# Kernel optimization log

Measured on AMD Instinct MI355X. Metric: run time of the kernel, lower is better.

## Reference

```python
import jax, jax.numpy as jnp
import numpy as np

BETA = 0.9
THRESHOLD = 1.0
SLOPE = 25.0


def _heaviside(x):
    return (x > 0).astype(x.dtype)


def setup_inputs() -> dict:
    key = jax.random.key(0)
    k = jax.random.split(key, 5)
    B, T, I, H, C = 256, 500, 256, 512, 8
    x = jax.random.normal(k[0], (B, T, I), dtype=jnp.float32)
    W1 = jax.random.normal(k[1], (H, I), dtype=jnp.float32) * (1.0 / np.sqrt(I))
    b1 = jax.random.normal(k[2], (H,), dtype=jnp.float32) * 0.01
    W2 = jax.random.normal(k[3], (C, H), dtype=jnp.float32) * (1.0 / np.sqrt(H))
    b2 = jax.random.normal(k[4], (C,), dtype=jnp.float32) * 0.01
    return {"x": x, "W1": W1, "b1": b1, "W2": W2, "b2": b2}


def reference(x, W1, b1, W2, b2):
    # x: (B, T, I)
    B, T, I = x.shape
    # Time-invariant fc1 batched outside the recurrence: (B, T, H)
    cur1 = jnp.einsum('bti,hi->bth', x, W1) + b1
    cur1_t = jnp.swapaxes(cur1, 0, 1)  # (T, B, H)

    def step(mem, cur):
        # snntorch Leaky (reset_mechanism='subtract'):
        # reset computed from previous mem crossing threshold
        reset = _heaviside(mem - THRESHOLD)
        mem_new = BETA * mem + cur - reset * THRESHOLD
        spk = _heaviside(mem_new - THRESHOLD)
        return mem_new, spk

    mem0 = jnp.zeros((B, W1.shape[0]), dtype=x.dtype)
    _, spks = jax.lax.scan(step, mem0, cur1_t)  # spks: (T, B, H)

    # out_sum = sum_t (spk_t @ W2^T + b2) = (sum_t spk_t) @ W2^T + T*b2
    spk_sum = spks.sum(axis=0)  # (B, H)
    out_sum = spk_sum @ W2.T + jnp.asarray(T, x.dtype) * b2  # (B, C)
    return out_sum
```

## Files before the change

### kernel.cpp

```cpp
#include <hip/hip_runtime.h>


#define B_   256
#define T_   500
#define I_   256
#define H_   512
#define C_   8

#define TC   128
#define BK   32
#define NKS  8
#define NCH  4
#define NR   (NCH * NKS)

#define WBUF  0
#define XBUF0 32768
#define XBUF1 49152

typedef __attribute__((ext_vector_type(8))) _Float16 half8;
typedef __attribute__((ext_vector_type(2))) __fp16 f16x2;
typedef __attribute__((ext_vector_type(4))) float f32x4;

typedef __attribute__((address_space(1))) const unsigned int as1_uint;
typedef __attribute__((address_space(3))) unsigned int as3_uint;

__device__ __forceinline__ void lds_dma16(const void* g, void* l) {
  __builtin_amdgcn_global_load_lds((as1_uint*)g, (as3_uint*)l, 16, 0, 0);
}

#define MFMA16(A, B, Cc) __builtin_amdgcn_mfma_f32_16x16x32_f16(A, B, Cc, 0, 0, 0)

__global__ void init_out_kernel(const float* __restrict__ b2,
                                float* __restrict__ out) {
  int idx = blockIdx.x * 256 + threadIdx.x;
  if (idx < B_ * C_) out[idx] = (float)T_ * b2[idx & (C_ - 1)];
}

__global__ void split_w1_kernel(const float* __restrict__ W1,
                                char* __restrict__ ws) {
  const int n = blockIdx.x * 256 + threadIdx.x;
  if (n >= H_ * NKS * 4) return;
  const int h = n >> 5, ks = (n >> 2) & 7, c = n & 3;
  const float* src = W1 + h * I_ + ks * BK + c * 8;
  union { half8 v; _Float16 e[8]; } hi, lo;
  #pragma unroll
  for (int e = 0; e < 8; ++e) {
    const float w = 16.0f * src[e];
    const _Float16 wh = (_Float16)w;
    hi.e[e] = wh;
    lo.e[e] = (_Float16)(w - (float)wh);
  }
  const int slot = (((h & 255) << 2) + c) ^ (h & 7);
  char* dst = ws + (size_t)((ks << 1) + (h >> 8)) * 32768 + ((size_t)slot << 4);
  *(half8*)dst = hi.v;
  *(half8*)(dst + 16384) = lo.v;
}

__device__ __forceinline__ void load_x16(const float* xb, int t, int ib,
                                         float* a) {
  if (t < T_) {
    const float* xr = xb + (size_t)t * I_ + ib;
    #pragma unroll
    for (int q = 0; q < 4; ++q) {
      const float4 v = *(const float4*)(xr + 4 * q);
      a[4 * q + 0] = v.x; a[4 * q + 1] = v.y;
      a[4 * q + 2] = v.z; a[4 * q + 3] = v.w;
    }
  } else {
    #pragma unroll
    for (int e = 0; e < 16; ++e) a[e] = 0.f;
  }
}

__device__ __forceinline__ void cvt_store_x(char* dstbase, int xs0, int xs1,
                                            const float* a) {
  union { half8 v; f16x2 p[4]; } h0, h1, l0, l1;
  #pragma unroll
  for (int k = 0; k < 4; ++k) {
    const f16x2 ha = __builtin_amdgcn_cvt_pkrtz(a[2 * k], a[2 * k + 1]);
    h0.p[k] = ha;
    l0.p[k] = __builtin_amdgcn_cvt_pkrtz(a[2 * k] - (float)ha[0],
                                         a[2 * k + 1] - (float)ha[1]);
    const f16x2 hb = __builtin_amdgcn_cvt_pkrtz(a[8 + 2 * k], a[9 + 2 * k]);
    h1.p[k] = hb;
    l1.p[k] = __builtin_amdgcn_cvt_pkrtz(a[8 + 2 * k] - (float)hb[0],
                                         a[9 + 2 * k] - (float)hb[1]);
  }
  *(half8*)(dstbase + xs0) = h0.v;
  *(half8*)(dstbase + xs1) = h1.v;
  *(half8*)(dstbase + 8192 + xs0) = l0.v;
  *(half8*)(dstbase + 8192 + xs1) = l1.v;
}

__global__ __launch_bounds__(256, 2) void snn_mfma2(
    const float* __restrict__ x, const char* __restrict__ ws,
    const float* __restrict__ b1, const float* __restrict__ W2,
    float* __restrict__ out) {
  __shared__ __align__(16) char smem[65536];

  const int tid = threadIdx.x;
  const int b = blockIdx.x, half = blockIdx.y;
  const int l = tid & 63, wv = tid >> 6;
  const int rr = l & 15, cc = l >> 4;

  const float* xb = x + (size_t)b * (T_ * I_);

  const int fsw = (((rr << 2) + cc) ^ (rr & 7)) << 4;

  const int tl = tid >> 1, ih = tid & 1;
  const int xs0 = ((((tl << 2) + ih * 2 + 0) ^ (tl & 7)) << 4);
  const int xs1 = ((((tl << 2) + ih * 2 + 1) ^ (tl & 7)) << 4);

  const float bias16 = 16.0f * b1[half * 256 + wv * 64 + l];
  float mreg = 0.f, cnt = 0.f;

  f32x4 acc[8][4];
  #pragma unroll
  for (int i = 0; i < 8; ++i)
    #pragma unroll
    for (int j = 0; j < 4; ++j) acc[i][j] = (f32x4){0.f, 0.f, 0.f, 0.f};

  {
    const char* wg = ws + (size_t)half * 32768;
    #pragma unroll
    for (int q = 0; q < 8; ++q)
      lds_dma16(wg + (wv * 8 + q) * 1024 + l * 16,
                smem + WBUF + (wv * 8 + q) * 1024);
    float a16[16];
    load_x16(xb, tl, ih * 16, a16);
    cvt_store_x(smem + XBUF0, xs0, xs1, a16);
    __syncthreads();
  }

  #pragma unroll 1
  for (int r = 0; r < NR; ++r) {
    const int ks = r & 7, chunk = r >> 3;
    const int xcur = XBUF0 + (r & 1) * 16384;
    const int xnxt = XBUF0 + ((r + 1) & 1) * 16384;
    const bool do_stage = (r + 1 < NR);

    float a16[16];
    if (do_stage) {
      const int t1 = ((r + 1) >> 3) * TC + tl;
      load_x16(xb, t1, ((r + 1) & 7) * BK + ih * 16, a16);
    }

    half8 ah[8], al[8], bh[4], bl[4];
    #pragma unroll
    for (int i = 0; i < 8; ++i) {
      ah[i] = *(const half8*)(smem + xcur + i * 1024 + fsw);
      al[i] = *(const half8*)(smem + xcur + 8192 + i * 1024 + fsw);
    }
    #pragma unroll
    for (int j = 0; j < 4; ++j) {
      bh[j] = *(const half8*)(smem + WBUF + wv * 4096 + j * 1024 + fsw);
      bl[j] = *(const half8*)(smem + WBUF + 16384 + wv * 4096 + j * 1024 + fsw);
    }
    #pragma unroll
    for (int i = 0; i < 8; ++i)
      #pragma unroll
      for (int j = 0; j < 4; ++j) {
        acc[i][j] = MFMA16(ah[i], bh[j], acc[i][j]);
        acc[i][j] = MFMA16(al[i], bh[j], acc[i][j]);
        acc[i][j] = MFMA16(ah[i], bl[j], acc[i][j]);
      }

    if (ks == 7) {
      asm volatile("" ::: "memory");
      const int t0 = chunk * TC;
      #pragma unroll
      for (int p = 0; p < 4; ++p) {
        #pragma unroll
        for (int i2 = 0; i2 < 2; ++i2) {
          #pragma unroll
          for (int j = 0; j < 4; ++j) {
            const int rl = j * 16 + rr;
            const int g = i2 * 4 + cc;
            const int ad = (rl >> 5) * 16384 + wv * 4096 + (rl & 31) * 128 +
                           ((g ^ (rl & 7)) << 4);
            *(f32x4*)(smem + ad) = acc[2 * p + i2][j];
          }
        }
        const int nt = T_ - (t0 + 32 * p) < 32 ? T_ - (t0 + 32 * p) : 32;
        const int rb = (l >> 5) * 16384 + wv * 4096 + (l & 31) * 128;
        #pragma unroll
        for (int g = 0; g < 8; ++g) {
          if (4 * g < nt) {
            const float4 v =
                *(const float4*)(smem + rb + ((g ^ (l & 7)) << 4));
            const float cv[4] = {v.x, v.y, v.z, v.w};
            #pragma unroll
            for (int e = 0; e < 4; ++e) {
              const float curv = cv[e] + bias16;
              const float rst = (mreg > 16.0f) ? 16.0f : 0.f;
              mreg = fmaf(0.9f, mreg, curv) - rst;
              if (mreg > 16.0f) cnt += 1.f;
            }
          }
        }
      }
      #pragma unroll
      for (int i = 0; i < 8; ++i)
        #pragma unroll
        for (int j = 0; j < 4; ++j) acc[i][j] = (f32x4){0.f, 0.f, 0.f, 0.f};
    }

    __syncthreads();

    if (do_stage) {
      const char* wg = ws + (size_t)((((r + 1) & 7) << 1) + half) * 32768;
      #pragma unroll
      for (int q = 0; q < 8; ++q)
        lds_dma16(wg + (wv * 8 + q) * 1024 + l * 16,
                  smem + WBUF + (wv * 8 + q) * 1024);
      cvt_store_x(smem + xnxt, xs0, xs1, a16);
    }
    __syncthreads();
  }

  const int hglob = half * 256 + wv * 64 + l;
  #pragma unroll
  for (int c = 0; c < C_; ++c) {
    float p = cnt * W2[c * H_ + hglob];
    #pragma unroll
    for (int m = 32; m >= 1; m >>= 1) p += __shfl_xor(p, m, 64);
    if (l == 0) atomicAdd(&out[b * C_ + c], p);
  }
}

extern "C" void kernel_launch(void* const* d_in, const int* in_sizes, int n_in,
                              void* d_out, int out_size, void* d_ws,
                              size_t ws_size, hipStream_t stream) {
  (void)in_sizes; (void)n_in; (void)ws_size; (void)out_size;
  const float* x  = (const float*)d_in[0];
  const float* W1 = (const float*)d_in[1];
  const float* b1 = (const float*)d_in[2];
  const float* W2 = (const float*)d_in[3];
  const float* b2 = (const float*)d_in[4];
  float* out = (float*)d_out;
  char* ws = (char*)d_ws;

  init_out_kernel<<<dim3((B_ * C_ + 255) / 256), dim3(256), 0, stream>>>(b2, out);
  split_w1_kernel<<<dim3(H_ * NKS * 4 / 256), dim3(256), 0, stream>>>(W1, ws);
  snn_mfma2<<<dim3(B_, 2), dim3(256), 0, stream>>>(x, ws, b1, W2, out);
}
```

Measured before the change: 261.2 us.

## Relayout W1 and x tiles to MFMA fragment order and fold bias into accumulators

W1 halves are pre-packed in the order the MFMA B fragments are read, and x tiles are staged so each lane writes and reads a contiguous 16-byte fragment. This removes the XOR swizzle arithmetic and lets the weight DMA use simple linear offsets. The bias is preloaded into the accumulators instead of being added in the scan. The membrane epilogue now processes 16 timesteps at a time through the idle next x buffer and tracks the spike flag in a register rather than re-comparing. Dropping the swizzle risks LDS bank conflicts on the epilogue stores.

```diff
diff --git a/kernel.cpp b/kernel.cpp
--- a/kernel.cpp
+++ b/kernel.cpp
@@ -40,7 +40,10 @@
                                 char* __restrict__ ws) {
   const int n = blockIdx.x * 256 + threadIdx.x;
   if (n >= H_ * NKS * 4) return;
-  const int h = n >> 5, ks = (n >> 2) & 7, c = n & 3;
+  const int blk = n >> 10, r = n & 1023;
+  const int ks = blk >> 1, hh = blk & 1;
+  const int h = hh * 256 + (r >> 8) * 64 + ((r >> 6) & 3) * 16 + (r & 15);
+  const int c = (r >> 4) & 3;
   const float* src = W1 + h * I_ + ks * BK + c * 8;
   union { half8 v; _Float16 e[8]; } hi, lo;
   #pragma unroll
@@ -50,111 +53,110 @@
     hi.e[e] = wh;
     lo.e[e] = (_Float16)(w - (float)wh);
   }
-  const int slot = (((h & 255) << 2) + c) ^ (h & 7);
-  char* dst = ws + (size_t)((ks << 1) + (h >> 8)) * 32768 + ((size_t)slot << 4);
+  char* dst = ws + (size_t)blk * 32768 + (size_t)r * 16;
   *(half8*)dst = hi.v;
   *(half8*)(dst + 16384) = lo.v;
 }
 
-__device__ __forceinline__ void load_x16(const float* xb, int t, int ib,
-                                         float* a) {
+__device__ __forceinline__ void load_x8(const float* xb, int t, int col,
+                                        float* a) {
   if (t < T_) {
-    const float* xr = xb + (size_t)t * I_ + ib;
-    #pragma unroll
-    for (int q = 0; q < 4; ++q) {
-      const float4 v = *(const float4*)(xr + 4 * q);
-      a[4 * q + 0] = v.x; a[4 * q + 1] = v.y;
-      a[4 * q + 2] = v.z; a[4 * q + 3] = v.w;
-    }
+    const float* p = xb + (size_t)t * I_ + col;
+    const float4 v0 = *(const float4*)p;
+    const float4 v1 = *(const float4*)(p + 4);
+    a[0] = v0.x; a[1] = v0.y; a[2] = v0.z; a[3] = v0.w;
+    a[4] = v1.x; a[5] = v1.y; a[6] = v1.z; a[7] = v1.w;
   } else {
     #pragma unroll
-    for (int e = 0; e < 16; ++e) a[e] = 0.f;
-  }
-}
-
-__device__ __forceinline__ void cvt_store_x(char* dstbase, int xs0, int xs1,
-                                            const float* a) {
-  union { half8 v; f16x2 p[4]; } h0, h1, l0, l1;
+    for (int e = 0; e < 8; ++e) a[e] = 0.f;
+  }
+}
+
+__device__ __forceinline__ void cvt_store(char* base, int tt, int l,
+                                          const float* a) {
+  union { half8 v; f16x2 p[4]; } h8, l8;
   #pragma unroll
   for (int k = 0; k < 4; ++k) {
     const f16x2 ha = __builtin_amdgcn_cvt_pkrtz(a[2 * k], a[2 * k + 1]);
-    h0.p[k] = ha;
-    l0.p[k] = __builtin_amdgcn_cvt_pkrtz(a[2 * k] - (float)ha[0],
+    h8.p[k] = ha;
+    l8.p[k] = __builtin_amdgcn_cvt_pkrtz(a[2 * k] - (float)ha[0],
                                          a[2 * k + 1] - (float)ha[1]);
-    const f16x2 hb = __builtin_amdgcn_cvt_pkrtz(a[8 + 2 * k], a[9 + 2 * k]);
-    h1.p[k] = hb;
-    l1.p[k] = __builtin_amdgcn_cvt_pkrtz(a[8 + 2 * k] - (float)hb[0],
-                                         a[9 + 2 * k] - (float)hb[1]);
-  }
-  *(half8*)(dstbase + xs0) = h0.v;
-  *(half8*)(dstbase + xs1) = h1.v;
-  *(half8*)(dstbase + 8192 + xs0) = l0.v;
-  *(half8*)(dstbase + 8192 + xs1) = l1.v;
-}
-
-__global__ __launch_bounds__(256, 2) void snn_mfma2(
+  }
+  *(half8*)(base + tt * 1024 + l * 16) = h8.v;
+  *(half8*)(base + 8192 + tt * 1024 + l * 16) = l8.v;
+}
+
+__global__ __launch_bounds__(256, 2) void snn_mfma3(
     const float* __restrict__ x, const char* __restrict__ ws,
     const float* __restrict__ b1, const float* __restrict__ W2,
     float* __restrict__ out) {
   __shared__ __align__(16) char smem[65536];
 
   const int tid = threadIdx.x;
-  const int b = blockIdx.x, half = blockIdx.y;
+  const int b = blockIdx.x, hf = blockIdx.y;
   const int l = tid & 63, wv = tid >> 6;
-  const int rr = l & 15, cc = l >> 4;
 
   const float* xb = x + (size_t)b * (T_ * I_);
 
-  const int fsw = (((rr << 2) + cc) ^ (rr & 7)) << 4;
-
-  const int tl = tid >> 1, ih = tid & 1;
-  const int xs0 = ((((tl << 2) + ih * 2 + 0) ^ (tl & 7)) << 4);
-  const int xs1 = ((((tl << 2) + ih * 2 + 1) ^ (tl & 7)) << 4);
-
-  const float bias16 = 16.0f * b1[half * 256 + wv * 64 + l];
+  const int xrow = l & 15;
+  const int xcolb = (l >> 4) * 8;
+
+  float biasj[4];
+  #pragma unroll
+  for (int j = 0; j < 4; ++j)
+    biasj[j] = 16.0f * b1[hf * 256 + wv * 64 + j * 16 + (l & 15)];
+
   float mreg = 0.f, cnt = 0.f;
+  bool sp = false;
 
   f32x4 acc[8][4];
   #pragma unroll
   for (int i = 0; i < 8; ++i)
     #pragma unroll
-    for (int j = 0; j < 4; ++j) acc[i][j] = (f32x4){0.f, 0.f, 0.f, 0.f};
+    for (int j = 0; j < 4; ++j)
+      acc[i][j] = (f32x4){biasj[j], biasj[j], biasj[j], biasj[j]};
 
   {
-    const char* wg = ws + (size_t)half * 32768;
-    #pragma unroll
-    for (int q = 0; q < 8; ++q)
-      lds_dma16(wg + (wv * 8 + q) * 1024 + l * 16,
-                smem + WBUF + (wv * 8 + q) * 1024);
-    float a16[16];
-    load_x16(xb, tl, ih * 16, a16);
-    cvt_store_x(smem + XBUF0, xs0, xs1, a16);
+    const char* wg = ws + (size_t)hf * 32768;
+    #pragma unroll
+    for (int q = 0; q < 4; ++q) {
+      const int o = (q * 256 + tid) * 16;
+      lds_dma16(wg + o, smem + WBUF + o);
+      lds_dma16(wg + 16384 + o, smem + WBUF + 16384 + o);
+    }
+    float a8[2][8];
+    load_x8(xb, 2 * wv * 16 + xrow, xcolb, a8[0]);
+    load_x8(xb, (2 * wv + 1) * 16 + xrow, xcolb, a8[1]);
+    cvt_store(smem + XBUF0, 2 * wv, l, a8[0]);
+    cvt_store(smem + XBUF0, 2 * wv + 1, l, a8[1]);
     __syncthreads();
   }
 
   #pragma unroll 1
   for (int r = 0; r < NR; ++r) {
-    const int ks = r & 7, chunk = r >> 3;
+    const int ks = r & 7;
     const int xcur = XBUF0 + (r & 1) * 16384;
     const int xnxt = XBUF0 + ((r + 1) & 1) * 16384;
     const bool do_stage = (r + 1 < NR);
 
-    float a16[16];
+    float a8[2][8];
     if (do_stage) {
-      const int t1 = ((r + 1) >> 3) * TC + tl;
-      load_x16(xb, t1, ((r + 1) & 7) * BK + ih * 16, a16);
+      const int t1 = ((r + 1) >> 3) * TC, c1 = ((r + 1) & 7) * BK + xcolb;
+      load_x8(xb, t1 + 2 * wv * 16 + xrow, c1, a8[0]);
+      load_x8(xb, t1 + (2 * wv + 1) * 16 + xrow, c1, a8[1]);
     }
 
     half8 ah[8], al[8], bh[4], bl[4];
     #pragma unroll
     for (int i = 0; i < 8; ++i) {
-      ah[i] = *(const half8*)(smem + xcur + i * 1024 + fsw);
-      al[i] = *(const half8*)(smem + xcur + 8192 + i * 1024 + fsw);
+      ah[i] = *(const half8*)(smem + xcur + i * 1024 + (l << 4));
+      al[i] = *(const half8*)(smem + xcur + 8192 + i * 1024 + (l << 4));
     }
     #pragma unroll
     for (int j = 0; j < 4; ++j) {
-      bh[j] = *(const half8*)(smem + WBUF + wv * 4096 + j * 1024 + fsw);
-      bl[j] = *(const half8*)(smem + WBUF + 16384 + wv * 4096 + j * 1024 + fsw);
+      bh[j] = *(const half8*)(smem + WBUF + (wv << 12) + (j << 10) + (l << 4));
+      bl[j] = *(const half8*)(smem + WBUF + 16384 + (wv << 12) + (j << 10) +
+                              (l << 4));
     }
     #pragma unroll
     for (int i = 0; i < 8; ++i)
@@ -167,34 +169,26 @@
 
     if (ks == 7) {
       asm volatile("" ::: "memory");
-      const int t0 = chunk * TC;
-      #pragma unroll
-      for (int p = 0; p < 4; ++p) {
+      const int t0 = (r >> 3) * TC;
+      char* dw = smem + xnxt + (wv << 12);
+      #pragma unroll
+      for (int p = 0; p < 8; ++p) {
         #pragma unroll
-        for (int i2 = 0; i2 < 2; ++i2) {
+        for (int j = 0; j < 4; ++j)
+          *(f32x4*)(dw + ((l >> 4) << 10) + (((j << 4) + (l & 15)) << 4)) =
+              acc[p][j];
+        const int tb = t0 + p * 16;
+        #pragma unroll
+        for (int g = 0; g < 4; ++g) {
+          const float4 v = *(const float4*)(dw + (g << 10) + (l << 4));
+          const float cv[4] = {v.x, v.y, v.z, v.w};
           #pragma unroll
-          for (int j = 0; j < 4; ++j) {
-            const int rl = j * 16 + rr;
-            const int g = i2 * 4 + cc;
-            const int ad = (rl >> 5) * 16384 + wv * 4096 + (rl & 31) * 128 +
-                           ((g ^ (rl & 7)) << 4);
-            *(f32x4*)(smem + ad) = acc[2 * p + i2][j];
-          }
-        }
-        const int nt = T_ - (t0 + 32 * p) < 32 ? T_ - (t0 + 32 * p) : 32;
-        const int rb = (l >> 5) * 16384 + wv * 4096 + (l & 31) * 128;
-        #pragma unroll
-        for (int g = 0; g < 8; ++g) {
-          if (4 * g < nt) {
-            const float4 v =
-                *(const float4*)(smem + rb + ((g ^ (l & 7)) << 4));
-            const float cv[4] = {v.x, v.y, v.z, v.w};
-            #pragma unroll
-            for (int e = 0; e < 4; ++e) {
-              const float curv = cv[e] + bias16;
-              const float rst = (mreg > 16.0f) ? 16.0f : 0.f;
-              mreg = fmaf(0.9f, mreg, curv) - rst;
-              if (mreg > 16.0f) cnt += 1.f;
+          for (int e = 0; e < 4; ++e) {
+            if (tb + g * 4 + e < T_) {
+              const float rst = sp ? 16.0f : 0.0f;
+              mreg = fmaf(0.9f, mreg, cv[e]) - rst;
+              sp = mreg > 16.0f;
+              if (sp) cnt += 1.0f;
             }
           }
         }
@@ -202,23 +196,27 @@
       #pragma unroll
       for (int i = 0; i < 8; ++i)
         #pragma unroll
-        for (int j = 0; j < 4; ++j) acc[i][j] = (f32x4){0.f, 0.f, 0.f, 0.f};
+        for (int j = 0; j < 4; ++j)
+          acc[i][j] = (f32x4){biasj[j], biasj[j], biasj[j], biasj[j]};
     }
 
     __syncthreads();
 
     if (do_stage) {
-      const char* wg = ws + (size_t)((((r + 1) & 7) << 1) + half) * 32768;
-      #pragma unroll
-      for (int q = 0; q < 8; ++q)
-        lds_dma16(wg + (wv * 8 + q) * 1024 + l * 16,
-                  smem + WBUF + (wv * 8 + q) * 1024);
-      cvt_store_x(smem + xnxt, xs0, xs1, a16);
+      const char* wg = ws + (size_t)((((r + 1) & 7) << 1) + hf) * 32768;
+      #pragma unroll
+      for (int q = 0; q < 4; ++q) {
+        const int o = (q * 256 + tid) * 16;
+        lds_dma16(wg + o, smem + WBUF + o);
+        lds_dma16(wg + 16384 + o, smem + WBUF + 16384 + o);
+      }
+      cvt_store(smem + xnxt, 2 * wv, l, a8[0]);
+      cvt_store(smem + xnxt, 2 * wv + 1, l, a8[1]);
     }
     __syncthreads();
   }
 
-  const int hglob = half * 256 + wv * 64 + l;
+  const int hglob = hf * 256 + wv * 64 + l;
   #pragma unroll
   for (int c = 0; c < C_; ++c) {
     float p = cnt * W2[c * H_ + hglob];
@@ -242,5 +240,5 @@
 
   init_out_kernel<<<dim3((B_ * C_ + 255) / 256), dim3(256), 0, stream>>>(b2, out);
   split_w1_kernel<<<dim3(H_ * NKS * 4 / 256), dim3(256), 0, stream>>>(W1, ws);
-  snn_mfma2<<<dim3(B_, 2), dim3(256), 0, stream>>>(x, ws, b1, W2, out);
-}
+  snn_mfma3<<<dim3(B_, 2), dim3(256), 0, stream>>>(x, ws, b1, W2, out);
+}
```

Result: faster. 249.6 us (-4.4%).
